# Optimization experiments

Hardware: AMD Instinct MI355X
Metric: run time of the kernel (lower is better)

Reference implementation:

```python
import jax, jax.numpy as jnp
from jax import lax
import numpy as np

N_RAYS = 524288
DIM = 3          # original space dim; extended space is DIM+1
HIDDEN = 128


def setup_inputs() -> dict:
    key = jax.random.key(0)
    k_r, k_p, k_w1, k_w2 = jax.random.split(key, 4)
    return {
        "r": jax.random.normal(k_r, (N_RAYS, DIM + 1), dtype=jnp.float32),
        "pivot": jax.random.normal(k_p, (1, DIM), dtype=jnp.float32),
        "W1": jax.random.normal(k_w1, (DIM, HIDDEN), dtype=jnp.float32),
        "b1": jnp.zeros((HIDDEN,), dtype=jnp.float32),
        "W2": jax.random.normal(k_w2, (HIDDEN, 1), dtype=jnp.float32),
        "b2": jnp.zeros((1,), dtype=jnp.float32),
        "n_iter": 20,
    }


def reference(r, pivot, W1, b1, W2, b2, n_iter):
    # neural SDF omega: (N, DIM) -> (N,)
    def sdf(x):
        h = jax.nn.softplus(x @ W1 + b1)   # (N, HIDDEN)
        return (h @ W2 + b2)[:, 0]         # (N,)

    # extended-space SDF with nu=None branch:
    # a = |s|; max(max(s, x0 - a), -a - x0)
    def ext_sdf(x):
        s = sdf(x[:, 1:])
        a = jnp.abs(s)
        x0 = x[:, 0]
        return jnp.maximum(jnp.maximum(s, x0 - a), -a - x0)

    # pivot lifted to extended space with leading zero coordinate: (1, DIM+1)
    pivot_ext = jnp.concatenate([jnp.zeros_like(pivot[:, :1]), pivot], axis=1)
    r_norm = r / jnp.linalg.norm(r, axis=1, keepdims=True)  # (N, DIM+1)

    # sphere tracing: from inside (sdf < 0), step alpha <- alpha - sdf(x)
    def step(alpha, _):
        x = pivot_ext + alpha[:, None] * r_norm
        return alpha - ext_sdf(x), None

    alpha0 = jnp.zeros((r.shape[0],), dtype=r.dtype)
    alpha, _ = lax.scan(step, alpha0, None, length=n_iter)

    res_x = pivot_ext + alpha[:, None] * r_norm   # (N, DIM+1)
    return res_x[:, 1:]                            # drop extended coordinate
```

## Files before the change

kernel.cpp:

```cpp
#include <hip/hip_runtime.h>
#include <math.h>

#define NRAYS      524288
#define HIDDEN     128
#define LOG2E_F    1.44269504088896340736f
#define LN2_F      0.69314718055994530942f
#define BUDGET_L2  89.0f
#define FULL_T     38

extern "C" __device__ float __ocml_native_exp2_f32(float);
extern "C" __device__ float __ocml_native_log2_f32(float);

typedef float f4v __attribute__((ext_vector_type(4)));
typedef int   i4v __attribute__((ext_vector_type(4)));

__device__ __forceinline__ float softplus2(float z) {
    const float e = __ocml_native_exp2_f32(-fabsf(z));
    return fmaxf(z, 0.0f) + __ocml_native_log2_f32(1.0f + e);
}

template <int CTRL, int ROW_MASK>
__device__ __forceinline__ float dpp_add(float v) {
    int t = __builtin_amdgcn_update_dpp(0, __builtin_bit_cast(int, v),
                                        CTRL, ROW_MASK, 0xf, true);
    return v + __builtin_bit_cast(float, t);
}
__device__ __forceinline__ float wave_sum_bcast(float v) {
    v = dpp_add<0x111, 0xf>(v);
    v = dpp_add<0x112, 0xf>(v);
    v = dpp_add<0x114, 0xf>(v);
    v = dpp_add<0x118, 0xf>(v);
    v = dpp_add<0x142, 0xa>(v);
    v = dpp_add<0x143, 0xc>(v);
    return __builtin_bit_cast(float,
        __builtin_amdgcn_readlane(__builtin_bit_cast(int, v), 63));
}
__device__ __forceinline__ float bcast_lane(float v, int l) {
    return __builtin_bit_cast(float,
        __builtin_amdgcn_readlane(__builtin_bit_cast(int, v), l));
}

__global__ void prep_kernel(const float* __restrict__ pivot,
                            const float* __restrict__ W1,
                            const float* __restrict__ b1,
                            const float* __restrict__ W2,
                            const float* __restrict__ b2,
                            float* __restrict__ ws) {
    __shared__ float part[2][6];
    const int j    = threadIdx.x;
    const int wv_w = j >> 6;
    const int lane = j & 63;
    const float w0 = W1[j], w1 = W1[HIDDEN + j], w2 = W1[2*HIDDEN + j];
    const float b1s = b1[j] * LOG2E_F;
    const float v   = W2[j] * LN2_F;
    const float ps0 = pivot[0]*LOG2E_F, ps1 = pivot[1]*LOG2E_F, ps2 = pivot[2]*LOG2E_F;
    const float c   = fmaf(ps0, w0, fmaf(ps1, w1, fmaf(ps2, w2, b1s)));
    const float vc  = v * c;
    ws[j]        = w0;
    ws[128 + j]  = w1;
    ws[256 + j]  = w2;
    ws[384 + j]  = v;
    ws[512 + j]  = vc;
    ws[640 + j]  = b1s;
    ((float4*)(ws + 768))[j] = make_float4(w0, w1, w2, v);

    const float sQa = wave_sum_bcast(vc);
    const float sQe = wave_sum_bcast(fabsf(vc) + fabsf(v));
    const float sS0 = wave_sum_bcast(softplus2(c) * v);
    const float sWx = wave_sum_bcast(v * w0);
    const float sWy = wave_sum_bcast(v * w1);
    const float sWz = wave_sum_bcast(v * w2);
    if (lane == 0) {
        part[wv_w][0] = sQa; part[wv_w][1] = sQe; part[wv_w][2] = sS0;
        part[wv_w][3] = sWx; part[wv_w][4] = sWy; part[wv_w][5] = sWz;
    }
    __syncthreads();
    if (j == 0) {
        ws[1280] = part[0][0] + part[1][0];
        ws[1281] = part[0][1] + part[1][1] + fabsf(b2[0]);
        ws[1282] = part[0][2] + part[1][2] + b2[0];
        ws[1283] = part[0][3] + part[1][3];
        ws[1284] = part[0][4] + part[1][4];
        ws[1285] = part[0][5] + part[1][5];
    }
}

__global__ __launch_bounds__(256) void raymarch_kernel(
    const float* __restrict__ r,
    const float* __restrict__ pivot,
    const float* __restrict__ b2,
    const int*   __restrict__ n_iter,
    const float* __restrict__ ws,
    float* __restrict__ out)
{
    const f4v* __restrict__ w0p = (const f4v*)(ws);
    const f4v* __restrict__ w1p = (const f4v*)(ws + 128);
    const f4v* __restrict__ w2p = (const f4v*)(ws + 256);
    const f4v* __restrict__ vpp = (const f4v*)(ws + 384);
    const f4v* __restrict__ vc4 = (const f4v*)(ws + 512);
    const float*  __restrict__ b1s = ws + 640;
    const float4* __restrict__ wv  = (const float4*)(ws + 768);

    const int i    = blockIdx.x * 256 + threadIdx.x;
    const int lane = threadIdx.x & 63;

    const float4 rv = ((const float4*)r)[i];
    const float inv = 1.0f / sqrtf(rv.x*rv.x + rv.y*rv.y + rv.z*rv.z + rv.w*rv.w);
    const float rn0 = rv.x*inv, rn1 = rv.y*inv, rn2 = rv.z*inv, rn3 = rv.w*inv;
    const float p0 = pivot[0], p1 = pivot[1], p2 = pivot[2];
    const float rs1 = rn1*LOG2E_F, rs2 = rn2*LOG2E_F, rs3 = rn3*LOG2E_F;
    const float ps0 = p0*LOG2E_F,  ps1 = p1*LOG2E_F,  ps2 = p2*LOG2E_F;
    const float bb2 = b2[0];
    const int   T   = n_iter[0];

    const float Qa   = ws[1280];
    const float Qesc = ws[1281];
    const float s0   = ws[1282];

    const float4 qa = wv[lane];
    const float4 qb = wv[64 + lane];
    const float  wa3 = b1s[lane], wb3 = b1s[64 + lane];

    auto part_ray = [&](float x1, float x2, float x3) -> float {
        const float z1 = fmaf(x1, qa.x, fmaf(x2, qa.y, fmaf(x3, qa.z, wa3)));
        const float z2 = fmaf(x1, qb.x, fmaf(x2, qb.y, fmaf(x3, qb.z, wb3)));
        return fmaf(softplus2(z1), qa.w, softplus2(z2) * qb.w);
    };

    const float Pa = fmaf(rs1, ws[1283], fmaf(rs2, ws[1284], rs3 * ws[1285]));
    f4v S1v = {0.f, 0.f, 0.f, 0.f}, S2v = {0.f, 0.f, 0.f, 0.f};
    const i4v SGN = {(int)0x80000000, (int)0x80000000,
                     (int)0x80000000, (int)0x80000000};
    #pragma unroll 8
    for (int k = 0; k < HIDDEN/4; ++k) {
        const f4v a0 = w0p[k], a1 = w1p[k], a2 = w2p[k];
        const f4v vv = vpp[k], vcp = vc4[k];
        const f4v d  = a0*rs1 + a1*rs2 + a2*rs3;
        const f4v vd = vv * d;
        const i4v sm = __builtin_bit_cast(i4v, d) & SGN;
        S1v += __builtin_bit_cast(f4v, __builtin_bit_cast(i4v, vd)  ^ sm);
        S2v += __builtin_bit_cast(f4v, __builtin_bit_cast(i4v, vcp) ^ sm);
    }
    const float S1 = (S1v.x + S1v.y) + (S1v.z + S1v.w);
    const float S2 = (S2v.x + S2v.y) + (S2v.z + S2v.w);

    const float Pp = 0.5f*(Pa + S1), Pm = 0.5f*(Pa - S1);
    const float Qp = 0.5f*(Qa + S2), Qm = 0.5f*(Qa - S2);
    const float Qpb = Qp + bb2, Qmb = Qm + bb2;

    const float Ph = fmaxf(fabsf(Pp), fabsf(Pm));
    const float M  = fmaxf(2.0f, 1.0f + fabsf(rn0) + Ph);
    const float Lm = __ocml_native_log2_f32(M);
    const float Le = __ocml_native_log2_f32(Qesc) + 1.0f;

    float alpha = (T > 0) ? -s0 : 0.0f;
    int t = 1;
    for (; t < T; ++t) {
        const bool need = fmaf((float)(T - 1 - t), Lm, Le) > BUDGET_L2;
        unsigned long long m = __ballot(need);
        if (m == 0ull) break;
        const bool pos = alpha > 0.0f;
        float s = fmaf(alpha, pos ? Pp : Pm, pos ? Qpb : Qmb);
        const float x1 = fmaf(alpha, rs1, ps0);
        const float x2 = fmaf(alpha, rs2, ps1);
        const float x3 = fmaf(alpha, rs3, ps2);
        if (__popcll(m) > FULL_T) {
            float acc = bb2;
            #pragma unroll 8
            for (int j = 0; j < HIDDEN; ++j) {
                const float4 q = wv[j];
                const float z = fmaf(x1, q.x,
                                fmaf(x2, q.y,
                                fmaf(x3, q.z, b1s[j])));
                acc = fmaf(softplus2(z), q.w, acc);
            }
            if (need) s = acc;
        } else {
            while (m) {
                const int l0 = (int)__ffsll(m) - 1;
                m &= m - 1;
                const float pa0 = part_ray(bcast_lane(x1, l0),
                                           bcast_lane(x2, l0),
                                           bcast_lane(x3, l0));
                if (m) {
                    const int l1 = (int)__ffsll(m) - 1;
                    m &= m - 1;
                    const float pa1 = part_ray(bcast_lane(x1, l1),
                                               bcast_lane(x2, l1),
                                               bcast_lane(x3, l1));
                    const float r0 = wave_sum_bcast(pa0) + bb2;
                    const float r1 = wave_sum_bcast(pa1) + bb2;
                    s = (lane == l0) ? r0 : ((lane == l1) ? r1 : s);
                } else {
                    const float r0 = wave_sum_bcast(pa0) + bb2;
                    s = (lane == l0) ? r0 : s;
                }
            }
        }
        const float a   = fabsf(s);
        const float x0  = alpha * rn0;
        alpha -= fmaxf(fmaxf(s, x0 - a), -a - x0);
    }
    for (; t < T; ++t) {
        const bool pos = alpha > 0.0f;
        const float s = fmaf(alpha, pos ? Pp : Pm, pos ? Qpb : Qmb);
        const float a   = fabsf(s);
        const float x0  = alpha * rn0;
        alpha -= fmaxf(fmaxf(s, x0 - a), -a - x0);
    }

    out[3*i + 0] = fmaf(alpha, rn1, p0);
    out[3*i + 1] = fmaf(alpha, rn2, p1);
    out[3*i + 2] = fmaf(alpha, rn3, p2);
}

extern "C" void kernel_launch(void* const* d_in, const int* in_sizes, int n_in,
                              void* d_out, int out_size, void* d_ws, size_t ws_size,
                              hipStream_t stream) {
    const float* r     = (const float*)d_in[0];
    const float* pivot = (const float*)d_in[1];
    const float* W1    = (const float*)d_in[2];
    const float* b1    = (const float*)d_in[3];
    const float* W2    = (const float*)d_in[4];
    const float* b2    = (const float*)d_in[5];
    const int*   nit   = (const int*)d_in[6];
    float* out = (float*)d_out;
    float* ws  = (float*)d_ws;

    prep_kernel<<<1, HIDDEN, 0, stream>>>(pivot, W1, b1, W2, b2, ws);
    raymarch_kernel<<<NRAYS / 256, 256, 0, stream>>>(r, pivot, b2, nit, ws, out);
}
```

Before: 92.70 us.

## Fold weight-prep kernel into raymarch kernel and drop dense full-wave path

Removes the separate single-block prep kernel and recomputes the prepared constants (bias-shifted weights, W2-weighted sums, softplus at pivot) inside every wave from the raw weights with DPP reductions. This saves one kernel launch and the serial dependency between the two kernels. In exchange each wave redoes the reductions and the S1/S2 loop now also computes the pivot term per ray. The dense per-lane 128-neuron evaluation used when many lanes needed the network is also removed, so every iteration takes the lane-broadcast path, which may cost more when most lanes are active.

```diff
diff --git a/kernel.cpp b/kernel.cpp
--- a/kernel.cpp
+++ b/kernel.cpp
@@ -6,7 +6,6 @@
 #define LOG2E_F    1.44269504088896340736f
 #define LN2_F      0.69314718055994530942f
 #define BUDGET_L2  89.0f
-#define FULL_T     38
 
 extern "C" __device__ float __ocml_native_exp2_f32(float);
 extern "C" __device__ float __ocml_native_log2_f32(float);
@@ -40,66 +39,21 @@
         __builtin_amdgcn_readlane(__builtin_bit_cast(int, v), l));
 }
 
-__global__ void prep_kernel(const float* __restrict__ pivot,
-                            const float* __restrict__ W1,
-                            const float* __restrict__ b1,
-                            const float* __restrict__ W2,
-                            const float* __restrict__ b2,
-                            float* __restrict__ ws) {
-    __shared__ float part[2][6];
-    const int j    = threadIdx.x;
-    const int wv_w = j >> 6;
-    const int lane = j & 63;
-    const float w0 = W1[j], w1 = W1[HIDDEN + j], w2 = W1[2*HIDDEN + j];
-    const float b1s = b1[j] * LOG2E_F;
-    const float v   = W2[j] * LN2_F;
-    const float ps0 = pivot[0]*LOG2E_F, ps1 = pivot[1]*LOG2E_F, ps2 = pivot[2]*LOG2E_F;
-    const float c   = fmaf(ps0, w0, fmaf(ps1, w1, fmaf(ps2, w2, b1s)));
-    const float vc  = v * c;
-    ws[j]        = w0;
-    ws[128 + j]  = w1;
-    ws[256 + j]  = w2;
-    ws[384 + j]  = v;
-    ws[512 + j]  = vc;
-    ws[640 + j]  = b1s;
-    ((float4*)(ws + 768))[j] = make_float4(w0, w1, w2, v);
-
-    const float sQa = wave_sum_bcast(vc);
-    const float sQe = wave_sum_bcast(fabsf(vc) + fabsf(v));
-    const float sS0 = wave_sum_bcast(softplus2(c) * v);
-    const float sWx = wave_sum_bcast(v * w0);
-    const float sWy = wave_sum_bcast(v * w1);
-    const float sWz = wave_sum_bcast(v * w2);
-    if (lane == 0) {
-        part[wv_w][0] = sQa; part[wv_w][1] = sQe; part[wv_w][2] = sS0;
-        part[wv_w][3] = sWx; part[wv_w][4] = sWy; part[wv_w][5] = sWz;
-    }
-    __syncthreads();
-    if (j == 0) {
-        ws[1280] = part[0][0] + part[1][0];
-        ws[1281] = part[0][1] + part[1][1] + fabsf(b2[0]);
-        ws[1282] = part[0][2] + part[1][2] + b2[0];
-        ws[1283] = part[0][3] + part[1][3];
-        ws[1284] = part[0][4] + part[1][4];
-        ws[1285] = part[0][5] + part[1][5];
-    }
-}
-
 __global__ __launch_bounds__(256) void raymarch_kernel(
     const float* __restrict__ r,
     const float* __restrict__ pivot,
+    const float* __restrict__ W1,
+    const float* __restrict__ b1,
+    const float* __restrict__ W2,
     const float* __restrict__ b2,
     const int*   __restrict__ n_iter,
-    const float* __restrict__ ws,
     float* __restrict__ out)
 {
-    const f4v* __restrict__ w0p = (const f4v*)(ws);
-    const f4v* __restrict__ w1p = (const f4v*)(ws + 128);
-    const f4v* __restrict__ w2p = (const f4v*)(ws + 256);
-    const f4v* __restrict__ vpp = (const f4v*)(ws + 384);
-    const f4v* __restrict__ vc4 = (const f4v*)(ws + 512);
-    const float*  __restrict__ b1s = ws + 640;
-    const float4* __restrict__ wv  = (const float4*)(ws + 768);
+    const f4v* __restrict__ w0p = (const f4v*)(W1);
+    const f4v* __restrict__ w1p = (const f4v*)(W1 + 128);
+    const f4v* __restrict__ w2p = (const f4v*)(W1 + 256);
+    const f4v* __restrict__ b1p = (const f4v*)(b1);
+    const f4v* __restrict__ v4p = (const f4v*)(W2);
 
     const int i    = blockIdx.x * 256 + threadIdx.x;
     const int lane = threadIdx.x & 63;
@@ -113,33 +67,45 @@
     const float bb2 = b2[0];
     const int   T   = n_iter[0];
 
-    const float Qa   = ws[1280];
-    const float Qesc = ws[1281];
-    const float s0   = ws[1282];
+    const float ua0 = W1[lane],      ua1 = W1[128+lane],    ua2 = W1[256+lane];
+    const float ub0 = W1[64+lane],   ub1 = W1[192+lane],    ub2 = W1[320+lane];
+    const float b1a = b1[lane],      b1b = b1[64+lane];
+    const float va  = W2[lane],      vb  = W2[64+lane];
+    const float b1as = b1a * LOG2E_F, b1bs = b1b * LOG2E_F;
+    const float val  = va * LN2_F,    vbl  = vb * LN2_F;
 
-    const float4 qa = wv[lane];
-    const float4 qb = wv[64 + lane];
-    const float  wa3 = b1s[lane], wb3 = b1s[64 + lane];
+    const float ca  = fmaf(p0, ua0, fmaf(p1, ua1, fmaf(p2, ua2, b1a)));
+    const float cb  = fmaf(p0, ub0, fmaf(p1, ub1, fmaf(p2, ub2, b1b)));
+    const float Qa   = wave_sum_bcast(fmaf(va, ca, vb * cb));
+    const float Qesc = wave_sum_bcast(fabsf(va*ca) + fabsf(vb*cb)
+                                      + fabsf(va) + fabsf(vb)) + fabsf(bb2);
+    const float s0   = wave_sum_bcast(
+        fmaf(softplus2(ca * LOG2E_F), val, softplus2(cb * LOG2E_F) * vbl)) + bb2;
+    const float Wvx  = wave_sum_bcast(fmaf(va, ua0, vb * ub0));
+    const float Wvy  = wave_sum_bcast(fmaf(va, ua1, vb * ub1));
+    const float Wvz  = wave_sum_bcast(fmaf(va, ua2, vb * ub2));
 
     auto part_ray = [&](float x1, float x2, float x3) -> float {
-        const float z1 = fmaf(x1, qa.x, fmaf(x2, qa.y, fmaf(x3, qa.z, wa3)));
-        const float z2 = fmaf(x1, qb.x, fmaf(x2, qb.y, fmaf(x3, qb.z, wb3)));
-        return fmaf(softplus2(z1), qa.w, softplus2(z2) * qb.w);
+        const float z1 = fmaf(x1, ua0, fmaf(x2, ua1, fmaf(x3, ua2, b1as)));
+        const float z2 = fmaf(x1, ub0, fmaf(x2, ub1, fmaf(x3, ub2, b1bs)));
+        return fmaf(softplus2(z1), val, softplus2(z2) * vbl);
     };
 
-    const float Pa = fmaf(rs1, ws[1283], fmaf(rs2, ws[1284], rs3 * ws[1285]));
+    const float Pa = fmaf(rn1, Wvx, fmaf(rn2, Wvy, rn3 * Wvz));
     f4v S1v = {0.f, 0.f, 0.f, 0.f}, S2v = {0.f, 0.f, 0.f, 0.f};
     const i4v SGN = {(int)0x80000000, (int)0x80000000,
                      (int)0x80000000, (int)0x80000000};
     #pragma unroll 8
     for (int k = 0; k < HIDDEN/4; ++k) {
         const f4v a0 = w0p[k], a1 = w1p[k], a2 = w2p[k];
-        const f4v vv = vpp[k], vcp = vc4[k];
-        const f4v d  = a0*rs1 + a1*rs2 + a2*rs3;
+        const f4v vv = v4p[k], bb = b1p[k];
+        const f4v d  = a0*rn1 + a1*rn2 + a2*rn3;
+        const f4v c  = a0*p0 + a1*p1 + a2*p2 + bb;
         const f4v vd = vv * d;
+        const f4v vc = vv * c;
         const i4v sm = __builtin_bit_cast(i4v, d) & SGN;
-        S1v += __builtin_bit_cast(f4v, __builtin_bit_cast(i4v, vd)  ^ sm);
-        S2v += __builtin_bit_cast(f4v, __builtin_bit_cast(i4v, vcp) ^ sm);
+        S1v += __builtin_bit_cast(f4v, __builtin_bit_cast(i4v, vd) ^ sm);
+        S2v += __builtin_bit_cast(f4v, __builtin_bit_cast(i4v, vc) ^ sm);
     }
     const float S1 = (S1v.x + S1v.y) + (S1v.z + S1v.w);
     const float S2 = (S2v.x + S2v.y) + (S2v.z + S2v.w);
@@ -164,37 +130,24 @@
         const float x1 = fmaf(alpha, rs1, ps0);
         const float x2 = fmaf(alpha, rs2, ps1);
         const float x3 = fmaf(alpha, rs3, ps2);
-        if (__popcll(m) > FULL_T) {
-            float acc = bb2;
-            #pragma unroll 8
-            for (int j = 0; j < HIDDEN; ++j) {
-                const float4 q = wv[j];
-                const float z = fmaf(x1, q.x,
-                                fmaf(x2, q.y,
-                                fmaf(x3, q.z, b1s[j])));
-                acc = fmaf(softplus2(z), q.w, acc);
-            }
-            if (need) s = acc;
-        } else {
-            while (m) {
-                const int l0 = (int)__ffsll(m) - 1;
+        while (m) {
+            const int l0 = (int)__ffsll(m) - 1;
+            m &= m - 1;
+            const float pa0 = part_ray(bcast_lane(x1, l0),
+                                       bcast_lane(x2, l0),
+                                       bcast_lane(x3, l0));
+            if (m) {
+                const int l1 = (int)__ffsll(m) - 1;
                 m &= m - 1;
-                const float pa0 = part_ray(bcast_lane(x1, l0),
-                                           bcast_lane(x2, l0),
-                                           bcast_lane(x3, l0));
-                if (m) {
-                    const int l1 = (int)__ffsll(m) - 1;
-                    m &= m - 1;
-                    const float pa1 = part_ray(bcast_lane(x1, l1),
-                                               bcast_lane(x2, l1),
-                                               bcast_lane(x3, l1));
-                    const float r0 = wave_sum_bcast(pa0) + bb2;
-                    const float r1 = wave_sum_bcast(pa1) + bb2;
-                    s = (lane == l0) ? r0 : ((lane == l1) ? r1 : s);
-                } else {
-                    const float r0 = wave_sum_bcast(pa0) + bb2;
-                    s = (lane == l0) ? r0 : s;
-                }
+                const float pa1 = part_ray(bcast_lane(x1, l1),
+                                           bcast_lane(x2, l1),
+                                           bcast_lane(x3, l1));
+                const float r0 = wave_sum_bcast(pa0) + bb2;
+                const float r1 = wave_sum_bcast(pa1) + bb2;
+                s = (lane == l0) ? r0 : ((lane == l1) ? r1 : s);
+            } else {
+                const float r0 = wave_sum_bcast(pa0) + bb2;
+                s = (lane == l0) ? r0 : s;
             }
         }
         const float a   = fabsf(s);
@@ -225,8 +178,7 @@
     const float* b2    = (const float*)d_in[5];
     const int*   nit   = (const int*)d_in[6];
     float* out = (float*)d_out;
-    float* ws  = (float*)d_ws;
 
-    prep_kernel<<<1, HIDDEN, 0, stream>>>(pivot, W1, b1, W2, b2, ws);
-    raymarch_kernel<<<NRAYS / 256, 256, 0, stream>>>(r, pivot, b2, nit, ws, out);
+    raymarch_kernel<<<NRAYS / 256, 256, 0, stream>>>(r, pivot, W1, b1, W2, b2,
+                                                     nit, out);
 }
```

After: 99.84 us. +7.7%, slower.

## Process two rays per thread to share weight loads and halve grid size

Applied to the files above, without the earlier changes.

Each thread now handles two rays (grid halved), so the hidden-layer weight loads in the setup loop and the full MLP evaluation are shared by two independent computations, which also adds instruction-level parallelism. The per-iteration budget test is precomputed into a per-ray end iteration (tEnd) so the loop only compares against t. The cost is more registers per thread, lower occupancy, and the wave-level full/partial choice now depends on the combined active count, so one slot can force full evaluation for the other.

```diff
diff --git a/kernel.cpp b/kernel.cpp
--- a/kernel.cpp
+++ b/kernel.cpp
@@ -85,6 +85,14 @@
     }
 }
 
+struct Ray {
+    float rn0, rn1, rn2, rn3;
+    float rs1, rs2, rs3;
+    float Pp, Pm, Qpb, Qmb;
+    float tEnd;
+    float alpha;
+};
+
 __global__ __launch_bounds__(256) void raymarch_kernel(
     const float* __restrict__ r,
     const float* __restrict__ pivot,
@@ -101,21 +109,19 @@
     const float*  __restrict__ b1s = ws + 640;
     const float4* __restrict__ wv  = (const float4*)(ws + 768);
 
-    const int i    = blockIdx.x * 256 + threadIdx.x;
+    const int base = blockIdx.x * 512 + threadIdx.x;
     const int lane = threadIdx.x & 63;
 
-    const float4 rv = ((const float4*)r)[i];
-    const float inv = 1.0f / sqrtf(rv.x*rv.x + rv.y*rv.y + rv.z*rv.z + rv.w*rv.w);
-    const float rn0 = rv.x*inv, rn1 = rv.y*inv, rn2 = rv.z*inv, rn3 = rv.w*inv;
     const float p0 = pivot[0], p1 = pivot[1], p2 = pivot[2];
-    const float rs1 = rn1*LOG2E_F, rs2 = rn2*LOG2E_F, rs3 = rn3*LOG2E_F;
-    const float ps0 = p0*LOG2E_F,  ps1 = p1*LOG2E_F,  ps2 = p2*LOG2E_F;
+    const float ps0 = p0*LOG2E_F, ps1 = p1*LOG2E_F, ps2 = p2*LOG2E_F;
     const float bb2 = b2[0];
     const int   T   = n_iter[0];
 
     const float Qa   = ws[1280];
     const float Qesc = ws[1281];
     const float s0   = ws[1282];
+    const float Wvx  = ws[1283], Wvy = ws[1284], Wvz = ws[1285];
+    const float Le   = __ocml_native_log2_f32(Qesc) + 1.0f;
 
     const float4 qa = wv[lane];
     const float4 qb = wv[64 + lane];
@@ -127,91 +133,145 @@
         return fmaf(softplus2(z1), qa.w, softplus2(z2) * qb.w);
     };
 
-    const float Pa = fmaf(rs1, ws[1283], fmaf(rs2, ws[1284], rs3 * ws[1285]));
-    f4v S1v = {0.f, 0.f, 0.f, 0.f}, S2v = {0.f, 0.f, 0.f, 0.f};
+    Ray R[2];
+    #pragma unroll
+    for (int slot = 0; slot < 2; ++slot) {
+        const float4 rv = ((const float4*)r)[base + slot * 256];
+        const float inv = 1.0f / sqrtf(rv.x*rv.x + rv.y*rv.y + rv.z*rv.z + rv.w*rv.w);
+        R[slot].rn0 = rv.x*inv; R[slot].rn1 = rv.y*inv;
+        R[slot].rn2 = rv.z*inv; R[slot].rn3 = rv.w*inv;
+        R[slot].rs1 = R[slot].rn1*LOG2E_F;
+        R[slot].rs2 = R[slot].rn2*LOG2E_F;
+        R[slot].rs3 = R[slot].rn3*LOG2E_F;
+    }
+
+    f4v S1A = {0,0,0,0}, S2A = {0,0,0,0}, S1B = {0,0,0,0}, S2B = {0,0,0,0};
     const i4v SGN = {(int)0x80000000, (int)0x80000000,
                      (int)0x80000000, (int)0x80000000};
     #pragma unroll 8
     for (int k = 0; k < HIDDEN/4; ++k) {
         const f4v a0 = w0p[k], a1 = w1p[k], a2 = w2p[k];
         const f4v vv = vpp[k], vcp = vc4[k];
-        const f4v d  = a0*rs1 + a1*rs2 + a2*rs3;
-        const f4v vd = vv * d;
-        const i4v sm = __builtin_bit_cast(i4v, d) & SGN;
-        S1v += __builtin_bit_cast(f4v, __builtin_bit_cast(i4v, vd)  ^ sm);
-        S2v += __builtin_bit_cast(f4v, __builtin_bit_cast(i4v, vcp) ^ sm);
-    }
-    const float S1 = (S1v.x + S1v.y) + (S1v.z + S1v.w);
-    const float S2 = (S2v.x + S2v.y) + (S2v.z + S2v.w);
-
-    const float Pp = 0.5f*(Pa + S1), Pm = 0.5f*(Pa - S1);
-    const float Qp = 0.5f*(Qa + S2), Qm = 0.5f*(Qa - S2);
-    const float Qpb = Qp + bb2, Qmb = Qm + bb2;
-
-    const float Ph = fmaxf(fabsf(Pp), fabsf(Pm));
-    const float M  = fmaxf(2.0f, 1.0f + fabsf(rn0) + Ph);
-    const float Lm = __ocml_native_log2_f32(M);
-    const float Le = __ocml_native_log2_f32(Qesc) + 1.0f;
-
-    float alpha = (T > 0) ? -s0 : 0.0f;
+        const f4v dA  = a0*R[0].rs1 + a1*R[0].rs2 + a2*R[0].rs3;
+        const f4v vdA = vv * dA;
+        const i4v smA = __builtin_bit_cast(i4v, dA) & SGN;
+        S1A += __builtin_bit_cast(f4v, __builtin_bit_cast(i4v, vdA) ^ smA);
+        S2A += __builtin_bit_cast(f4v, __builtin_bit_cast(i4v, vcp) ^ smA);
+        const f4v dB  = a0*R[1].rs1 + a1*R[1].rs2 + a2*R[1].rs3;
+        const f4v vdB = vv * dB;
+        const i4v smB = __builtin_bit_cast(i4v, dB) & SGN;
+        S1B += __builtin_bit_cast(f4v, __builtin_bit_cast(i4v, vdB) ^ smB);
+        S2B += __builtin_bit_cast(f4v, __builtin_bit_cast(i4v, vcp) ^ smB);
+    }
+    #pragma unroll
+    for (int slot = 0; slot < 2; ++slot) {
+        const f4v S1v = slot ? S1B : S1A;
+        const f4v S2v = slot ? S2B : S2A;
+        const float S1 = (S1v.x + S1v.y) + (S1v.z + S1v.w);
+        const float S2 = (S2v.x + S2v.y) + (S2v.z + S2v.w);
+        const float Pa = fmaf(R[slot].rs1, Wvx,
+                         fmaf(R[slot].rs2, Wvy, R[slot].rs3 * Wvz));
+        R[slot].Pp  = 0.5f*(Pa + S1);
+        R[slot].Pm  = 0.5f*(Pa - S1);
+        R[slot].Qpb = 0.5f*(Qa + S2) + bb2;
+        R[slot].Qmb = 0.5f*(Qa - S2) + bb2;
+        const float Ph = fmaxf(fabsf(R[slot].Pp), fabsf(R[slot].Pm));
+        const float M  = fmaxf(2.0f, 1.0f + fabsf(R[slot].rn0) + Ph);
+        const float Lm = __ocml_native_log2_f32(M);
+        R[slot].tEnd  = (float)(T - 1) - __fdividef(BUDGET_L2 - Le, Lm);
+        R[slot].alpha = (T > 0) ? -s0 : 0.0f;
+    }
+
     int t = 1;
     for (; t < T; ++t) {
-        const bool need = fmaf((float)(T - 1 - t), Lm, Le) > BUDGET_L2;
-        unsigned long long m = __ballot(need);
-        if (m == 0ull) break;
-        const bool pos = alpha > 0.0f;
-        float s = fmaf(alpha, pos ? Pp : Pm, pos ? Qpb : Qmb);
-        const float x1 = fmaf(alpha, rs1, ps0);
-        const float x2 = fmaf(alpha, rs2, ps1);
-        const float x3 = fmaf(alpha, rs3, ps2);
-        if (__popcll(m) > FULL_T) {
-            float acc = bb2;
+        const bool needA = (float)t < R[0].tEnd;
+        const bool needB = (float)t < R[1].tEnd;
+        unsigned long long mA = __ballot(needA);
+        unsigned long long mB = __ballot(needB);
+        if ((mA | mB) == 0ull) break;
+        float sv[2];
+        float x1v[2], x2v[2], x3v[2];
+        #pragma unroll
+        for (int slot = 0; slot < 2; ++slot) {
+            const float al = R[slot].alpha;
+            const bool pos = al > 0.0f;
+            sv[slot] = fmaf(al, pos ? R[slot].Pp : R[slot].Pm,
+                                pos ? R[slot].Qpb : R[slot].Qmb);
+            x1v[slot] = fmaf(al, R[slot].rs1, ps0);
+            x2v[slot] = fmaf(al, R[slot].rs2, ps1);
+            x3v[slot] = fmaf(al, R[slot].rs3, ps2);
+        }
+        if (__popcll(mA) + __popcll(mB) > FULL_T) {
+            float accA = bb2, accB = bb2;
             #pragma unroll 8
             for (int j = 0; j < HIDDEN; ++j) {
                 const float4 q = wv[j];
-                const float z = fmaf(x1, q.x,
-                                fmaf(x2, q.y,
-                                fmaf(x3, q.z, b1s[j])));
-                acc = fmaf(softplus2(z), q.w, acc);
+                const float bj = b1s[j];
+                const float zA = fmaf(x1v[0], q.x,
+                                 fmaf(x2v[0], q.y, fmaf(x3v[0], q.z, bj)));
+                accA = fmaf(softplus2(zA), q.w, accA);
+                const float zB = fmaf(x1v[1], q.x,
+                                 fmaf(x2v[1], q.y, fmaf(x3v[1], q.z, bj)));
+                accB = fmaf(softplus2(zB), q.w, accB);
             }
-            if (need) s = acc;
+            if (needA) sv[0] = accA;
+            if (needB) sv[1] = accB;
         } else {
-            while (m) {
-                const int l0 = (int)__ffsll(m) - 1;
-                m &= m - 1;
-                const float pa0 = part_ray(bcast_lane(x1, l0),
-                                           bcast_lane(x2, l0),
-                                           bcast_lane(x3, l0));
-                if (m) {
-                    const int l1 = (int)__ffsll(m) - 1;
+            #pragma unroll
+            for (int slot = 0; slot < 2; ++slot) {
+                unsigned long long m = slot ? mB : mA;
+                const float X1 = x1v[slot], X2 = x2v[slot], X3 = x3v[slot];
+                while (m) {
+                    const int l0 = (int)__ffsll(m) - 1;
                     m &= m - 1;
-                    const float pa1 = part_ray(bcast_lane(x1, l1),
-                                               bcast_lane(x2, l1),
-                                               bcast_lane(x3, l1));
-                    const float r0 = wave_sum_bcast(pa0) + bb2;
-                    const float r1 = wave_sum_bcast(pa1) + bb2;
-                    s = (lane == l0) ? r0 : ((lane == l1) ? r1 : s);
-                } else {
-                    const float r0 = wave_sum_bcast(pa0) + bb2;
-                    s = (lane == l0) ? r0 : s;
+                    const float pa0 = part_ray(bcast_lane(X1, l0),
+                                               bcast_lane(X2, l0),
+                                               bcast_lane(X3, l0));
+                    if (m) {
+                        const int l1 = (int)__ffsll(m) - 1;
+                        m &= m - 1;
+                        const float pa1 = part_ray(bcast_lane(X1, l1),
+                                                   bcast_lane(X2, l1),
+                                                   bcast_lane(X3, l1));
+                        const float r0 = wave_sum_bcast(pa0) + bb2;
+                        const float r1 = wave_sum_bcast(pa1) + bb2;
+                        sv[slot] = (lane == l0) ? r0
+                                 : ((lane == l1) ? r1 : sv[slot]);
+                    } else {
+                        const float r0 = wave_sum_bcast(pa0) + bb2;
+                        sv[slot] = (lane == l0) ? r0 : sv[slot];
+                    }
                 }
             }
         }
-        const float a   = fabsf(s);
-        const float x0  = alpha * rn0;
-        alpha -= fmaxf(fmaxf(s, x0 - a), -a - x0);
+        #pragma unroll
+        for (int slot = 0; slot < 2; ++slot) {
+            const float s  = sv[slot];
+            const float a  = fabsf(s);
+            const float x0 = R[slot].alpha * R[slot].rn0;
+            R[slot].alpha -= fmaxf(fmaxf(s, x0 - a), -a - x0);
+        }
     }
     for (; t < T; ++t) {
-        const bool pos = alpha > 0.0f;
-        const float s = fmaf(alpha, pos ? Pp : Pm, pos ? Qpb : Qmb);
-        const float a   = fabsf(s);
-        const float x0  = alpha * rn0;
-        alpha -= fmaxf(fmaxf(s, x0 - a), -a - x0);
-    }
-
-    out[3*i + 0] = fmaf(alpha, rn1, p0);
-    out[3*i + 1] = fmaf(alpha, rn2, p1);
-    out[3*i + 2] = fmaf(alpha, rn3, p2);
+        #pragma unroll
+        for (int slot = 0; slot < 2; ++slot) {
+            const float al = R[slot].alpha;
+            const bool pos = al > 0.0f;
+            const float s = fmaf(al, pos ? R[slot].Pp : R[slot].Pm,
+                                     pos ? R[slot].Qpb : R[slot].Qmb);
+            const float a  = fabsf(s);
+            const float x0 = al * R[slot].rn0;
+            R[slot].alpha = al - fmaxf(fmaxf(s, x0 - a), -a - x0);
+        }
+    }
+
+    #pragma unroll
+    for (int slot = 0; slot < 2; ++slot) {
+        const int i = base + slot * 256;
+        out[3*i + 0] = fmaf(R[slot].alpha, R[slot].rn1, p0);
+        out[3*i + 1] = fmaf(R[slot].alpha, R[slot].rn2, p1);
+        out[3*i + 2] = fmaf(R[slot].alpha, R[slot].rn3, p2);
+    }
 }
 
 extern "C" void kernel_launch(void* const* d_in, const int* in_sizes, int n_in,
@@ -228,5 +288,5 @@
     float* ws  = (float*)d_ws;
 
     prep_kernel<<<1, HIDDEN, 0, stream>>>(pivot, W1, b1, W2, b2, ws);
-    raymarch_kernel<<<NRAYS / 256, 256, 0, stream>>>(r, pivot, b2, nit, ws, out);
-}
+    raymarch_kernel<<<NRAYS / 512, 256, 0, stream>>>(r, pivot, b2, nit, ws, out);
+}
```

Result: no change. 92.62 us (-0.1%).
